# Kernel optimization log

Hardware: AMD Instinct MI355X
Metric: run time of the kernel (lower is better)

The kernel has to match this reference:

```python
import jax, jax.numpy as jnp
import numpy as np

MAXV = 127.0  # 2**(8-1) - 1, signed int8 symmetric range


def setup_inputs() -> dict:
    key = jax.random.key(0)
    kx, kw, kb = jax.random.split(key, 3)
    x = jax.random.normal(kx, (4, 2048, 4096), dtype=jnp.float32)
    weight = jax.random.normal(kw, (4096, 4096), dtype=jnp.float32) * 0.02
    bias = jax.random.normal(kb, (4096,), dtype=jnp.float32) * 0.01
    return {"x": x, "weight": weight, "bias": bias}


def reference(x, weight, bias):
    # Per-tensor max calibration (TensorQuantizer.amax)
    amax_x = jnp.max(jnp.abs(x))
    amax_w = jnp.max(jnp.abs(weight))
    sx = MAXV / amax_x
    sw = MAXV / amax_w
    # Quantize to int8 (fake_quant=False path -> integer tensors)
    qx = jnp.clip(jnp.round(x * sx), -MAXV, MAXV).astype(jnp.int8)
    qw = jnp.clip(jnp.round(weight * sw), -MAXV, MAXV).astype(jnp.int8)
    # Exact systolic int8 MAC -> int32 accumulate: [b, s, out]
    out_i32 = jnp.matmul(
        qx.astype(jnp.int32), qw.astype(jnp.int32).T,
        preferred_element_type=jnp.int32,
    )
    # Dequantize and add bias
    out = out_i32.astype(jnp.float32) / (sx * sw) + bias
    return out
```

## Files before the change

### kernel.cpp

```cpp
#include <hip/hip_runtime.h>

#define MAXV 127.0f
#define Mdim 8192
#define Ndim 4096
#define Kdim 4096
#define BM 128
#define BN 128
#define BK 64

#define EW_GRID 2048
#define EW_BLOCK 256
#define EW_STRIDE (EW_GRID * EW_BLOCK)
#define NX4 (Mdim * Kdim / 4)
#define NW4 (Ndim * Kdim / 4)

typedef __attribute__((ext_vector_type(4))) int int32x4;

__device__ __forceinline__ void async_load16(const void* g, void* l) {
  __builtin_amdgcn_global_load_lds(
      (const __attribute__((address_space(1))) unsigned int*)g,
      (__attribute__((address_space(3))) unsigned int*)l, 16, 0, 0);
}

__device__ __forceinline__ float amax4(float4 v) {
  return fmaxf(fmaxf(fabsf(v.x), fabsf(v.y)), fmaxf(fabsf(v.z), fabsf(v.w)));
}

__global__ __launch_bounds__(EW_BLOCK) void amax_both_kernel(
    const float4* __restrict__ x, const float4* __restrict__ w,
    int* __restrict__ out_bits) {
  const int t = blockIdx.x * EW_BLOCK + threadIdx.x;
  float mx = 0.0f, mw = 0.0f;
#pragma unroll
  for (int i = 0; i < 4; i++) {
    float4 a = x[t + (4 * i + 0) * EW_STRIDE];
    float4 b = x[t + (4 * i + 1) * EW_STRIDE];
    float4 c = x[t + (4 * i + 2) * EW_STRIDE];
    float4 d = x[t + (4 * i + 3) * EW_STRIDE];
    mx = fmaxf(mx, fmaxf(fmaxf(amax4(a), amax4(b)), fmaxf(amax4(c), amax4(d))));
  }
#pragma unroll
  for (int i = 0; i < 2; i++) {
    float4 a = w[t + (4 * i + 0) * EW_STRIDE];
    float4 b = w[t + (4 * i + 1) * EW_STRIDE];
    float4 c = w[t + (4 * i + 2) * EW_STRIDE];
    float4 d = w[t + (4 * i + 3) * EW_STRIDE];
    mw = fmaxf(mw, fmaxf(fmaxf(amax4(a), amax4(b)), fmaxf(amax4(c), amax4(d))));
  }
  for (int off = 32; off > 0; off >>= 1) {
    mx = fmaxf(mx, __shfl_down(mx, off));
    mw = fmaxf(mw, __shfl_down(mw, off));
  }
  __shared__ float sm[8];
  if ((threadIdx.x & 63) == 0) {
    sm[threadIdx.x >> 6] = mx;
    sm[4 + (threadIdx.x >> 6)] = mw;
  }
  __syncthreads();
  if (threadIdx.x == 0) {
    atomicMax(out_bits,
              __float_as_int(fmaxf(fmaxf(sm[0], sm[1]), fmaxf(sm[2], sm[3]))));
    atomicMax(out_bits + 1,
              __float_as_int(fmaxf(fmaxf(sm[4], sm[5]), fmaxf(sm[6], sm[7]))));
  }
}

__device__ __forceinline__ char4 quant4(float4 v, float s) {
  char4 q;
  q.x = (signed char)(int)fminf(fmaxf(rintf(v.x * s), -MAXV), MAXV);
  q.y = (signed char)(int)fminf(fmaxf(rintf(v.y * s), -MAXV), MAXV);
  q.z = (signed char)(int)fminf(fmaxf(rintf(v.z * s), -MAXV), MAXV);
  q.w = (signed char)(int)fminf(fmaxf(rintf(v.w * s), -MAXV), MAXV);
  return q;
}

__global__ __launch_bounds__(EW_BLOCK) void quant_both_kernel(
    const float4* __restrict__ x, const float4* __restrict__ w,
    const int* __restrict__ amax_bits, char4* __restrict__ qx,
    char4* __restrict__ qw) {
  const float sx = MAXV / __int_as_float(amax_bits[0]);
  const float sw = MAXV / __int_as_float(amax_bits[1]);
  const int t = blockIdx.x * EW_BLOCK + threadIdx.x;
#pragma unroll
  for (int i = 0; i < 4; i++) {
    int i0 = t + (4 * i + 0) * EW_STRIDE, i1 = t + (4 * i + 1) * EW_STRIDE;
    int i2 = t + (4 * i + 2) * EW_STRIDE, i3 = t + (4 * i + 3) * EW_STRIDE;
    float4 a = x[i0], b = x[i1], c = x[i2], d = x[i3];
    qx[i0] = quant4(a, sx);
    qx[i1] = quant4(b, sx);
    qx[i2] = quant4(c, sx);
    qx[i3] = quant4(d, sx);
  }
#pragma unroll
  for (int i = 0; i < 2; i++) {
    int i0 = t + (4 * i + 0) * EW_STRIDE, i1 = t + (4 * i + 1) * EW_STRIDE;
    int i2 = t + (4 * i + 2) * EW_STRIDE, i3 = t + (4 * i + 3) * EW_STRIDE;
    float4 a = w[i0], b = w[i1], c = w[i2], d = w[i3];
    qw[i0] = quant4(a, sw);
    qw[i1] = quant4(b, sw);
    qw[i2] = quant4(c, sw);
    qw[i3] = quant4(d, sw);
  }
}

__global__ __launch_bounds__(256) void gemm_i8_kernel(
    const signed char* __restrict__ Aq, const signed char* __restrict__ Bq,
    const float* __restrict__ bias, const int* __restrict__ amax_bits,
    float* __restrict__ out) {
  __shared__ signed char As[BM * BK];
  __shared__ signed char Bs[BN * BK];

  const int tid = threadIdx.x;
  const int lane = tid & 63;
  const int w = tid >> 6;
  const int wm = w >> 1;
  const int wn = w & 1;

  const int m0 = blockIdx.y * BM;
  const int n0 = blockIdx.x * BN;

  int32x4 acc[4][4] = {};

  const signed char* Abase =
      Aq + (size_t)(m0 + (tid >> 2)) * Kdim + (tid & 3) * 16;
  const signed char* Bbase =
      Bq + (size_t)(n0 + (tid >> 2)) * Kdim + (tid & 3) * 16;
  const size_t rowskip = (size_t)64 * Kdim;

  const int aoff = (wm * 64 + (lane & 15)) * BK + (lane >> 4) * 16;
  const int boff = (wn * 64 + (lane & 15)) * BK + (lane >> 4) * 16;

  for (int k0 = 0; k0 < Kdim; k0 += BK) {
    async_load16(Abase + k0, &As[w * 1024]);
    async_load16(Abase + rowskip + k0, &As[4096 + w * 1024]);
    async_load16(Bbase + k0, &Bs[w * 1024]);
    async_load16(Bbase + rowskip + k0, &Bs[4096 + w * 1024]);
    __syncthreads();

    int32x4 a[4], b[4];
#pragma unroll
    for (int i = 0; i < 4; i++)
      a[i] = *(const int32x4*)&As[aoff + i * 16 * BK];
#pragma unroll
    for (int j = 0; j < 4; j++)
      b[j] = *(const int32x4*)&Bs[boff + j * 16 * BK];

#pragma unroll
    for (int i = 0; i < 4; i++)
#pragma unroll
      for (int j = 0; j < 4; j++)
        acc[i][j] =
            __builtin_amdgcn_mfma_i32_16x16x64_i8(a[i], b[j], acc[i][j], 0, 0, 0);
    __syncthreads();
  }

  const float sx = MAXV / __int_as_float(amax_bits[0]);
  const float sw = MAXV / __int_as_float(amax_bits[1]);
  const float inv = 1.0f / (sx * sw);
  const int crow = (lane >> 4) * 4;
  const int ccol = lane & 15;
#pragma unroll
  for (int j = 0; j < 4; j++) {
    const int n = n0 + wn * 64 + j * 16 + ccol;
    const float bv = bias[n];
#pragma unroll
    for (int i = 0; i < 4; i++) {
      const int m = m0 + wm * 64 + i * 16 + crow;
      float* op = out + (size_t)m * Ndim + n;
#pragma unroll
      for (int r = 0; r < 4; r++)
        op[(size_t)r * Ndim] = (float)acc[i][j][r] * inv + bv;
    }
  }
}

extern "C" void kernel_launch(void* const* d_in, const int* in_sizes, int n_in,
                              void* d_out, int out_size, void* d_ws,
                              size_t ws_size, hipStream_t stream) {
  const float* x = (const float*)d_in[0];
  const float* wgt = (const float*)d_in[1];
  const float* bias = (const float*)d_in[2];
  float* out = (float*)d_out;

  int* amax = (int*)d_ws;
  signed char* qx = (signed char*)d_ws + 256;
  signed char* qw = qx + (size_t)Mdim * Kdim;

  hipMemsetAsync(amax, 0, 2 * sizeof(int), stream);
  hipLaunchKernelGGL(amax_both_kernel, dim3(EW_GRID), dim3(EW_BLOCK), 0, stream,
                     (const float4*)x, (const float4*)wgt, amax);
  hipLaunchKernelGGL(quant_both_kernel, dim3(EW_GRID), dim3(EW_BLOCK), 0,
                     stream, (const float4*)x, (const float4*)wgt, amax,
                     (char4*)qx, (char4*)qw);
  hipLaunchKernelGGL(gemm_i8_kernel, dim3(Ndim / BN, Mdim / BM), dim3(256), 0,
                     stream, qx, qw, bias, amax, out);
}
```

Measured before the change: 477.8 us.

## Rewrite int8 GEMM as 256x256 tiled, double-buffered, swizzled LDS pipeline

Replaces the simple 128x128 single-buffered int8 GEMM with a 256x256 tile using 512 threads (8 waves), BK=128, double-buffered LDS filled by async global-to-LDS loads, and XOR-swizzled LDS addressing. The main loop is split into phases that interleave staging the next K-tile with MFMA work, using explicit barriers, waitcnts and setprio. The aim is to hide global-load latency, avoid LDS bank conflicts and raise MFMA utilisation through more reuse per tile. In exchange it uses much more LDS (128KB per block) and more registers, which limits occupancy, and the hand-scheduled waitcnt counts are fragile.

```diff
diff --git a/kernel.cpp b/kernel.cpp
--- a/kernel.cpp
+++ b/kernel.cpp
@@ -4,15 +4,10 @@
 #define Mdim 8192
 #define Ndim 4096
 #define Kdim 4096
-#define BM 128
-#define BN 128
-#define BK 64
 
 #define EW_GRID 2048
 #define EW_BLOCK 256
 #define EW_STRIDE (EW_GRID * EW_BLOCK)
-#define NX4 (Mdim * Kdim / 4)
-#define NW4 (Ndim * Kdim / 4)
 
 typedef __attribute__((ext_vector_type(4))) int int32x4;
 
@@ -103,55 +98,148 @@
   }
 }
 
-__global__ __launch_bounds__(256) void gemm_i8_kernel(
+#define BM 256
+#define BN 256
+#define BKB 128
+#define HALF 16384
+#define NIT 15
+
+#define LDSA(buf) (lds + ((buf) * 4 + wm) * HALF)
+#define LDSB(buf) (lds + ((buf) * 4 + 2 + (wn >> 1)) * HALF)
+
+#define STG_A(buf, h, kt)                                          \
+  {                                                                \
+    signed char* d = lds + ((buf) * 4 + (h)) * HALF + wdst;        \
+    const signed char* s = aS + (h) * HSK + (size_t)(kt) * BKB;    \
+    async_load16(s, d);                                            \
+    async_load16(s + 64 * (size_t)Kdim, d + 8192);                 \
+  }
+#define STG_B(buf, h, kt)                                          \
+  {                                                                \
+    signed char* d = lds + ((buf) * 4 + 2 + (h)) * HALF + wdst;    \
+    const signed char* s = bS + (h) * HSK + (size_t)(kt) * BKB;    \
+    async_load16(s, d);                                            \
+    async_load16(s + 64 * (size_t)Kdim, d + 8192);                 \
+  }
+
+#define LOAD_A(buf, mh)                                            \
+  {                                                                \
+    const signed char* ab = LDSA(buf) + (mh) * 8192;               \
+    _Pragma("unroll") for (int mi = 0; mi < 4; mi++) {             \
+      afr[mi][0] = *(const int32x4*)(ab + mi * 2048 + aoff0);      \
+      afr[mi][1] = *(const int32x4*)(ab + mi * 2048 + aoff1);      \
+    }                                                              \
+  }
+#define LOAD_B(buf, g)                                             \
+  {                                                                \
+    const signed char* bb = LDSB(buf) + brow0 + (g) * 4096;        \
+    _Pragma("unroll") for (int j = 0; j < 2; j++) {                \
+      bfr[(g) * 2 + j][0] = *(const int32x4*)(bb + j * 2048 + aoff0); \
+      bfr[(g) * 2 + j][1] = *(const int32x4*)(bb + j * 2048 + aoff1); \
+    }                                                              \
+  }
+
+#define MFMA_Q(ma, nb)                                                        \
+  _Pragma("unroll") for (int mi = 0; mi < 4; mi++)                            \
+  _Pragma("unroll") for (int nj = 0; nj < 2; nj++)                            \
+  _Pragma("unroll") for (int ks = 0; ks < 2; ks++)                            \
+      acc[(ma) * 4 + mi][(nb) * 2 + nj] =                                     \
+          __builtin_amdgcn_mfma_i32_16x16x64_i8(                              \
+              afr[mi][ks], bfr[(nb) * 2 + nj][ks],                            \
+              acc[(ma) * 4 + mi][(nb) * 2 + nj], 0, 0, 0);
+
+#define SYNC_MID()                                       \
+  __builtin_amdgcn_s_barrier();                          \
+  asm volatile("s_waitcnt lgkmcnt(0)" ::: "memory");     \
+  __builtin_amdgcn_sched_barrier(0);                     \
+  __builtin_amdgcn_s_setprio(1);
+
+#define PH_END()                \
+  __builtin_amdgcn_s_setprio(0); \
+  __builtin_amdgcn_s_barrier();
+
+#define PH_END_V(n)                                      \
+  __builtin_amdgcn_s_setprio(0);                         \
+  asm volatile("s_waitcnt vmcnt(" #n ")" ::: "memory");  \
+  __builtin_amdgcn_s_barrier();
+
+__global__ __launch_bounds__(512, 2) void gemm_i8_kernel(
     const signed char* __restrict__ Aq, const signed char* __restrict__ Bq,
     const float* __restrict__ bias, const int* __restrict__ amax_bits,
     float* __restrict__ out) {
-  __shared__ signed char As[BM * BK];
-  __shared__ signed char Bs[BN * BK];
+  __shared__ signed char lds[8 * HALF];
 
   const int tid = threadIdx.x;
   const int lane = tid & 63;
   const int w = tid >> 6;
-  const int wm = w >> 1;
-  const int wn = w & 1;
+  const int wm = w >> 2;
+  const int wn = w & 3;
 
   const int m0 = blockIdx.y * BM;
   const int n0 = blockIdx.x * BN;
 
-  int32x4 acc[4][4] = {};
-
-  const signed char* Abase =
-      Aq + (size_t)(m0 + (tid >> 2)) * Kdim + (tid & 3) * 16;
-  const signed char* Bbase =
-      Bq + (size_t)(n0 + (tid >> 2)) * Kdim + (tid & 3) * 16;
-  const size_t rowskip = (size_t)64 * Kdim;
-
-  const int aoff = (wm * 64 + (lane & 15)) * BK + (lane >> 4) * 16;
-  const int boff = (wn * 64 + (lane & 15)) * BK + (lane >> 4) * 16;
-
-  for (int k0 = 0; k0 < Kdim; k0 += BK) {
-    async_load16(Abase + k0, &As[w * 1024]);
-    async_load16(Abase + rowskip + k0, &As[4096 + w * 1024]);
-    async_load16(Bbase + k0, &Bs[w * 1024]);
-    async_load16(Bbase + rowskip + k0, &Bs[4096 + w * 1024]);
-    __syncthreads();
-
-    int32x4 a[4], b[4];
-#pragma unroll
-    for (int i = 0; i < 4; i++)
-      a[i] = *(const int32x4*)&As[aoff + i * 16 * BK];
-#pragma unroll
-    for (int j = 0; j < 4; j++)
-      b[j] = *(const int32x4*)&Bs[boff + j * 16 * BK];
-
-#pragma unroll
-    for (int i = 0; i < 4; i++)
-#pragma unroll
-      for (int j = 0; j < 4; j++)
-        acc[i][j] =
-            __builtin_amdgcn_mfma_i32_16x16x64_i8(a[i], b[j], acc[i][j], 0, 0, 0);
-    __syncthreads();
+  const int r0 = tid >> 3;
+  const int gcol = ((tid & 7) * 16) ^ ((r0 & 7) << 4);
+  const signed char* aS = Aq + (size_t)(m0 + r0) * Kdim + gcol;
+  const signed char* bS = Bq + (size_t)(n0 + r0) * Kdim + gcol;
+  const size_t HSK = (size_t)128 * Kdim;
+  const int wdst = w * 1024;
+
+  const int aoff0 =
+      (lane & 15) * 128 + (((lane >> 4) * 16) ^ ((lane & 7) << 4));
+  const int aoff1 =
+      (lane & 15) * 128 + ((64 + (lane >> 4) * 16) ^ ((lane & 7) << 4));
+  const int brow0 = (wn & 1) * 8192;
+
+  int32x4 acc[8][4] = {};
+  int32x4 afr[4][2], bfr[4][2];
+
+  STG_A(0, 0, 0);
+  STG_A(0, 1, 0);
+  STG_B(0, 0, 0);
+  STG_B(0, 1, 0);
+  STG_B(1, 0, 1);
+  STG_B(1, 1, 1);
+  asm volatile("s_waitcnt vmcnt(4)" ::: "memory");
+  __builtin_amdgcn_s_barrier();
+
+#pragma unroll 1
+  for (int it = 0; it < NIT; ++it) {
+    const int kt1 = 2 * it + 1, kt2 = 2 * it + 2, kt3 = 2 * it + 3;
+    LOAD_A(0, 0); LOAD_B(0, 0); STG_A(1, 0, kt1);
+    SYNC_MID(); MFMA_Q(0, 0); PH_END();
+    LOAD_B(0, 1); STG_A(1, 1, kt1);
+    SYNC_MID(); MFMA_Q(0, 1); PH_END();
+    LOAD_A(0, 1); STG_B(0, 0, kt2);
+    SYNC_MID(); MFMA_Q(1, 1); PH_END();
+    STG_B(0, 1, kt2);
+    SYNC_MID(); MFMA_Q(1, 0); PH_END_V(4);
+    LOAD_A(1, 0); LOAD_B(1, 0); STG_A(0, 0, kt2);
+    SYNC_MID(); MFMA_Q(0, 0); PH_END();
+    LOAD_B(1, 1); STG_A(0, 1, kt2);
+    SYNC_MID(); MFMA_Q(0, 1); PH_END();
+    LOAD_A(1, 1); STG_B(1, 0, kt3);
+    SYNC_MID(); MFMA_Q(1, 1); PH_END();
+    STG_B(1, 1, kt3);
+    SYNC_MID(); MFMA_Q(1, 0); PH_END_V(4);
+  }
+
+  {
+    LOAD_A(0, 0); LOAD_B(0, 0); STG_A(1, 0, 31);
+    SYNC_MID(); MFMA_Q(0, 0); PH_END();
+    LOAD_B(0, 1); STG_A(1, 1, 31);
+    SYNC_MID(); MFMA_Q(0, 1); PH_END();
+    LOAD_A(0, 1);
+    SYNC_MID(); MFMA_Q(1, 1); PH_END();
+    SYNC_MID(); MFMA_Q(1, 0); PH_END_V(0);
+    LOAD_A(1, 0); LOAD_B(1, 0);
+    SYNC_MID(); MFMA_Q(0, 0); PH_END();
+    LOAD_B(1, 1);
+    SYNC_MID(); MFMA_Q(0, 1); PH_END();
+    LOAD_A(1, 1);
+    SYNC_MID(); MFMA_Q(1, 1); PH_END();
+    SYNC_MID(); MFMA_Q(1, 0);
+    __builtin_amdgcn_s_setprio(0);
   }
 
   const float sx = MAXV / __int_as_float(amax_bits[0]);
@@ -160,16 +248,16 @@
   const int crow = (lane >> 4) * 4;
   const int ccol = lane & 15;
 #pragma unroll
-  for (int j = 0; j < 4; j++) {
-    const int n = n0 + wn * 64 + j * 16 + ccol;
+  for (int nj = 0; nj < 4; nj++) {
+    const int n = n0 + wn * 64 + nj * 16 + ccol;
     const float bv = bias[n];
 #pragma unroll
-    for (int i = 0; i < 4; i++) {
-      const int m = m0 + wm * 64 + i * 16 + crow;
+    for (int a = 0; a < 8; a++) {
+      const int m = m0 + wm * 128 + a * 16 + crow;
       float* op = out + (size_t)m * Ndim + n;
 #pragma unroll
       for (int r = 0; r < 4; r++)
-        op[(size_t)r * Ndim] = (float)acc[i][j][r] * inv + bv;
+        op[(size_t)r * Ndim] = (float)acc[a][nj][r] * inv + bv;
     }
   }
 }
@@ -192,6 +280,6 @@
   hipLaunchKernelGGL(quant_both_kernel, dim3(EW_GRID), dim3(EW_BLOCK), 0,
                      stream, (const float4*)x, (const float4*)wgt, amax,
                      (char4*)qx, (char4*)qw);
-  hipLaunchKernelGGL(gemm_i8_kernel, dim3(Ndim / BN, Mdim / BM), dim3(256), 0,
+  hipLaunchKernelGGL(gemm_i8_kernel, dim3(Ndim / BN, Mdim / BM), dim3(512), 0,
                      stream, qx, qw, bias, amax, out);
 }
```

After: 430.0 us. 10.0% less time.
